# Optimization experiments

Measured on AMD Instinct MI355X. Metric: run time of the kernel, lower is better.

Reference implementation:

```python
import jax, jax.numpy as jnp
import numpy as np

B, T, P, C = 1, 256, 88, 128   # batch, time frames, 88 piano pitches, hidden_per_pitch
HEADS, WIN, NLAYERS = 4, 25, 2
HD = C // HEADS


def setup_inputs() -> dict:
    ks = jax.random.split(jax.random.key(0), 8)
    s = 0.02
    return {
        "x": jax.random.normal(ks[0], (B, T, P, C), jnp.float32),
        "condition": jax.random.normal(ks[1], (B, T, P, 2), jnp.float32),
        "mask": jax.random.uniform(ks[2], (B, T, P), jnp.float32),
        # fusion linear: Linear(hidden_per_pitch + 3, hidden_per_pitch)
        "linear_w": jax.random.normal(ks[3], (C, C + 3), jnp.float32) * s,
        "linear_b": jnp.zeros((C,), jnp.float32),
        # shared NeighborhoodAttention2D params (nn.Sequential repeats the same module)
        "qkv_w": jax.random.normal(ks[4], (3 * C, C), jnp.float32) * s,
        "qkv_b": jnp.zeros((3 * C,), jnp.float32),
        "rpb": jax.random.normal(ks[5], (HEADS, 2 * WIN - 1, 2 * WIN - 1), jnp.float32) * s,
        "proj_w": jax.random.normal(ks[6], (C, C), jnp.float32) * s,
        "proj_b": jnp.zeros((C,), jnp.float32),
    }


def _nbr_idx(n, w):
    # NATTEN edge-clamped windows: window start is clamped so every query sees w keys.
    start = jnp.clip(jnp.arange(n) - (w - 1) // 2, 0, n - w)
    idx = start[:, None] + jnp.arange(w)             # [n, w] absolute key indices
    rel = idx - jnp.arange(n)[:, None] + (w - 1)     # [n, w] rpb indices in [0, 2w-2]
    return idx, rel


def na2d(x, qkv_w, qkv_b, rpb, proj_w, proj_b):
    b, h, w_, c = x.shape
    qkv = (x @ qkv_w.T + qkv_b).reshape(b, h, w_, 3, HEADS, HD)
    q, k, v = (jnp.moveaxis(qkv[..., i, :, :], 3, 1) for i in range(3))  # [b,heads,h,w,hd]
    q = q * (HD ** -0.5)

    idx_h, rel_h = _nbr_idx(h, WIN)
    idx_w, rel_w = _nbr_idx(w_, WIN)

    def score_step(_, ki):
        kg = k[:, :, idx_h[:, ki]][:, :, :, idx_w]
        s = jnp.einsum('bhijd,bhijkd->bhijk', q, kg)
        s = s + rpb[:, rel_h[:, ki]][:, :, rel_w][None]
        return None, s

    _, scores = jax.lax.scan(score_step, None, jnp.arange(WIN))
    scores = jnp.moveaxis(scores, 0, 4)
    attn = jax.nn.softmax(scores.reshape(b, HEADS, h, w_, WIN * WIN), axis=-1)
    attn = attn.reshape(b, HEADS, h, w_, WIN, WIN)

    def out_step(acc, ki):
        vg = v[:, :, idx_h[:, ki]][:, :, :, idx_w]
        return acc + jnp.einsum('bhijk,bhijkd->bhijd', attn[..., ki, :], vg), None

    out, _ = jax.lax.scan(out_step, jnp.zeros_like(q), jnp.arange(WIN))
    out = jnp.moveaxis(out, 1, 3).reshape(b, h, w_, c)      # merge heads
    return out @ proj_w.T + proj_b


def reference(x, condition, mask, linear_w, linear_b, qkv_w, qkv_b, rpb, proj_w, proj_b):
    cat = jnp.concatenate([x, condition, mask[..., None]], axis=-1)  # [B,T,P,C+3]
    y = jax.nn.relu(cat @ linear_w.T + linear_b)
    for _ in range(NLAYERS):  # same module repeated -> shared weights
        y = na2d(y, qkv_w, qkv_b, rpb, proj_w, proj_b)
    return y
```

## Files before the change

### kernel.cpp

```cpp
#include <hip/hip_runtime.h>
#include <hip/hip_fp16.h>

#define TT 256
#define PP 88
#define CC 128
#define NN (TT * PP)
#define HEADS 4
#define HD 32
#define WIN 25
#define RPBW 49
#define RPBSZ (RPBW * RPBW)
#define SCALE 0.17677669529663687f
#define LOG2E 1.4426950408889634f
#define QSC (SCALE * LOG2E)

#define KVROW 11264
#define KVAARWS 258

#if __has_builtin(__builtin_amdgcn_exp2f)
#define EXP2(x) __builtin_amdgcn_exp2f(x)
#else
#define EXP2(x) exp2f(x)
#endif

typedef _Float16 f16;
typedef f16 f16x8 __attribute__((ext_vector_type(8)));
typedef f16 f16x8u __attribute__((ext_vector_type(8), aligned(4)));
typedef f16 f16x4 __attribute__((ext_vector_type(4)));
typedef f16 f16x4u __attribute__((ext_vector_type(4), aligned(4)));
typedef float f32x4 __attribute__((ext_vector_type(4)));
typedef float f32x4u __attribute__((ext_vector_type(4), aligned(4)));
typedef __fp16 hf16x2 __attribute__((ext_vector_type(2)));
union PkU { hf16x2 h; unsigned u; };

__global__ __launch_bounds__(256) void prep(
    const float* __restrict__ lw, const float* __restrict__ qw,
    const float* __restrict__ pw, const float* __restrict__ qb,
    const float* __restrict__ pb, const float* __restrict__ rpb,
    f16* __restrict__ lwh, f16* __restrict__ qwh, f16* __restrict__ pwh,
    f16* __restrict__ w2h, float* __restrict__ qbs, float* __restrict__ b2s,
    float* __restrict__ rpbp)
{
    const int b = blockIdx.x;
    if (b < 192) {
        int idx = b * 256 + threadIdx.x;
        if (idx < 128 * 160) {
            int r = idx / 160, c = idx - r * 160;
            lwh[idx] = (f16)(c < 131 ? lw[r * 131 + c] : 0.f);
        }
        if (idx < 384 * 128) {
            float v = qw[idx];
            if (idx < 128 * 128) v *= QSC;
            qwh[idx] = (f16)v;
        }
        if (idx < 128 * 128) pwh[idx] = (f16)pw[idx];
        if (idx < 384) qbs[idx] = qb[idx] * (idx < 128 ? QSC : 1.f);
        if (idx < 10240) rpbp[idx] = (idx < 4 * RPBSZ) ? rpb[idx] * LOG2E : 0.f;
    } else if (b < 216) {
        int t = (b - 192) * 256 + threadIdx.x;
        int i = t >> 4, l = t & 15;
        if (i < 384) {
            float s = 0.f;
            #pragma unroll
            for (int j = l * 8; j < l * 8 + 8; j++) s += qw[i * 128 + j] * pb[j];
            s += __shfl_xor(s, 1); s += __shfl_xor(s, 2);
            s += __shfl_xor(s, 4); s += __shfl_xor(s, 8);
            if (l == 0) b2s[i] = (qb[i] + s) * (i < 128 ? QSC : 1.f);
        }
    } else {
        const int bw = b - 216;
        const int m0 = (bw & 1) * 64;
        const int n0 = (bw >> 1) * 64;
        const int tid = threadIdx.x;
        const int w = tid >> 6, lane = tid & 63, quad = lane >> 4, nn = lane & 15;
        const int krow = m0 + w * 16 + nn;
        f16x8 af[4];
        #pragma unroll
        for (int ks = 0; ks < 4; ks++) {
            union { f16 e[8]; f16x8 v; } t;
            #pragma unroll
            for (int e = 0; e < 8; e++)
                t.e[e] = (f16)pw[(ks * 32 + quad * 8 + e) * 128 + krow];
            af[ks] = t.v;
        }
        f32x4 acc[4] = {};
        #pragma unroll
        for (int nt = 0; nt < 4; nt++) {
            int irow = n0 + nt * 16 + nn;
            #pragma unroll
            for (int ks = 0; ks < 4; ks++) {
                const float* qr = &qw[(size_t)irow * 128 + ks * 32 + quad * 8];
                float4 a = *(const float4*)qr, bq = *(const float4*)(qr + 4);
                PkU u0, u1, u2, u3;
                u0.h = __builtin_amdgcn_cvt_pkrtz(a.x, a.y);
                u1.h = __builtin_amdgcn_cvt_pkrtz(a.z, a.w);
                u2.h = __builtin_amdgcn_cvt_pkrtz(bq.x, bq.y);
                u3.h = __builtin_amdgcn_cvt_pkrtz(bq.z, bq.w);
                union { unsigned u[4]; f16x8 v; } bb;
                bb.u[0] = u0.u; bb.u[1] = u1.u; bb.u[2] = u2.u; bb.u[3] = u3.u;
                acc[nt] = __builtin_amdgcn_mfma_f32_16x16x32_f16(af[ks], bb.v, acc[nt], 0, 0, 0);
            }
        }
        #pragma unroll
        for (int nt = 0; nt < 4; nt++) {
            int i = n0 + nt * 16 + nn;
            float sc = (i < 128) ? QSC : 1.f;
            PkU p0, p1;
            p0.h = __builtin_amdgcn_cvt_pkrtz(acc[nt][0] * sc, acc[nt][1] * sc);
            p1.h = __builtin_amdgcn_cvt_pkrtz(acc[nt][2] * sc, acc[nt][3] * sc);
            *(uint2*)&w2h[(size_t)i * 128 + m0 + w * 16 + quad * 4] = make_uint2(p0.u, p1.u);
        }
    }
}

__global__ __launch_bounds__(256) void fusion_gemm(
    const float* __restrict__ x, const float* __restrict__ cond, const float* __restrict__ mask,
    const f16* __restrict__ lwh, const float* __restrict__ lb, f16* __restrict__ yh)
{
    __shared__ __align__(16) f16 Alds[64 * 168];
    const int m0 = blockIdx.x * 64, n0 = blockIdx.y * 64;
    const int tid = threadIdx.x;
    const int w = tid >> 6, lane = tid & 63, quad = lane >> 4, nn = lane & 15;

    {
        int r = tid >> 2, cpart = tid & 3;
        size_t pos = m0 + r;
        *(uint4*)&Alds[r * 168 + 128 + cpart * 8] = make_uint4(0, 0, 0, 0);
        const float* xr = x + pos * 128 + cpart * 32;
        #pragma unroll
        for (int t = 0; t < 4; t++) {
            float4 a = *(const float4*)(xr + t * 8);
            float4 b = *(const float4*)(xr + t * 8 + 4);
            PkU p0, p1, p2, p3;
            p0.h = __builtin_amdgcn_cvt_pkrtz(a.x, a.y);
            p1.h = __builtin_amdgcn_cvt_pkrtz(a.z, a.w);
            p2.h = __builtin_amdgcn_cvt_pkrtz(b.x, b.y);
            p3.h = __builtin_amdgcn_cvt_pkrtz(b.z, b.w);
            *(uint4*)&Alds[r * 168 + cpart * 32 + t * 8] = make_uint4(p0.u, p1.u, p2.u, p3.u);
        }
        if (cpart == 0) {
            Alds[r * 168 + 128] = (f16)cond[pos * 2];
            Alds[r * 168 + 129] = (f16)cond[pos * 2 + 1];
            Alds[r * 168 + 130] = (f16)mask[pos];
        }
    }
    __syncthreads();

    const int oc = n0 + w * 16 + nn;
    f16x8 af[5];
    #pragma unroll
    for (int ks = 0; ks < 5; ks++)
        af[ks] = *(const f16x8*)&lwh[(size_t)oc * 160 + ks * 32 + quad * 8];
    f32x4 acc[4] = {};
    #pragma unroll
    for (int ks = 0; ks < 5; ks++)
        #pragma unroll
        for (int nt = 0; nt < 4; nt++) {
            f16x8 bf = *(const f16x8*)&Alds[(nt * 16 + nn) * 168 + ks * 32 + quad * 8];
            acc[nt] = __builtin_amdgcn_mfma_f32_16x16x32_f16(af[ks], bf, acc[nt], 0, 0, 0);
        }
    float bv[4];
    #pragma unroll
    for (int r = 0; r < 4; r++) bv[r] = lb[n0 + w * 16 + quad * 4 + r];
    #pragma unroll
    for (int nt = 0; nt < 4; nt++) {
        int pos = m0 + nt * 16 + nn;
        PkU p0, p1;
        p0.h = __builtin_amdgcn_cvt_pkrtz(fmaxf(acc[nt][0] + bv[0], 0.f), fmaxf(acc[nt][1] + bv[1], 0.f));
        p1.h = __builtin_amdgcn_cvt_pkrtz(fmaxf(acc[nt][2] + bv[2], 0.f), fmaxf(acc[nt][3] + bv[3], 0.f));
        *(uint2*)&yh[(size_t)pos * 128 + n0 + w * 16 + quad * 4] = make_uint2(p0.u, p1.u);
    }
}

__global__ __launch_bounds__(256) void gemm_qkv(
    const f16* __restrict__ A, const f16* __restrict__ W, const float* __restrict__ bias,
    f16* __restrict__ qh, f16* __restrict__ kh2, f16* __restrict__ vh2)
{
    __shared__ __align__(16) f16 Alds[64 * 136];
    const int m0 = blockIdx.x * 64, n0 = blockIdx.y * 64;
    const int tid = threadIdx.x;
    const int w = tid >> 6, lane = tid & 63, quad = lane >> 4, nn = lane & 15;

    for (int i = tid; i < 1024; i += 256) {
        int r = i >> 4, c = i & 15;
        *(uint4*)&Alds[r * 136 + c * 8] = *(const uint4*)&A[(size_t)(m0 + r) * 128 + c * 8];
    }
    __syncthreads();

    const int oc = n0 + w * 16 + nn;
    f16x8 af[4];
    #pragma unroll
    for (int ks = 0; ks < 4; ks++)
        af[ks] = *(const f16x8*)&W[(size_t)oc * 128 + ks * 32 + quad * 8];
    f32x4 acc[4] = {};
    #pragma unroll
    for (int ks = 0; ks < 4; ks++)
        #pragma unroll
        for (int nt = 0; nt < 4; nt++) {
            f16x8 bf = *(const f16x8*)&Alds[(nt * 16 + nn) * 136 + ks * 32 + quad * 8];
            acc[nt] = __builtin_amdgcn_mfma_f32_16x16x32_f16(af[ks], bf, acc[nt], 0, 0, 0);
        }
    float bv[4];
    #pragma unroll
    for (int r = 0; r < 4; r++) bv[r] = bias[n0 + w * 16 + quad * 4 + r];

    if (n0 < 128) {
        #pragma unroll
        for (int nt = 0; nt < 4; nt++) {
            int pos = m0 + nt * 16 + nn;
            PkU p0, p1;
            p0.h = __builtin_amdgcn_cvt_pkrtz(acc[nt][0] + bv[0], acc[nt][1] + bv[1]);
            p1.h = __builtin_amdgcn_cvt_pkrtz(acc[nt][2] + bv[2], acc[nt][3] + bv[3]);
            *(uint2*)&qh[(size_t)pos * 128 + n0 + w * 16 + quad * 4] = make_uint2(p0.u, p1.u);
        }
    } else if (n0 < 256) {
        const int ch = n0 - 128 + w * 16 + quad * 4;
        const int hh = ch >> 5, c32 = ch & 31;
        #pragma unroll
        for (int nt = 0; nt < 4; nt++) {
            int pos = m0 + nt * 16 + nn;
            int aa = pos / 88, j = pos - aa * 88;
            PkU p0, p1;
            p0.h = __builtin_amdgcn_cvt_pkrtz(acc[nt][0] + bv[0], acc[nt][1] + bv[1]);
            p1.h = __builtin_amdgcn_cvt_pkrtz(acc[nt][2] + bv[2], acc[nt][3] + bv[3]);
            *(uint2*)&kh2[((size_t)(aa * 4 + hh) * 88 + j) * 32 + c32] = make_uint2(p0.u, p1.u);
        }
    } else {
        const int chb = n0 - 256 + w * 16 + quad * 4;
        #pragma unroll
        for (int nt = 0; nt < 4; nt++) {
            int pos = m0 + nt * 16 + nn;
            int aa = pos / 88, j = pos - aa * 88;
            size_t vb = (size_t)(aa * 4) * 2816 + (j >> 2) * 64 + (j & 3);
            #pragma unroll
            for (int r = 0; r < 4; r++) {
                int chg = chb + r;
                int hh = chg >> 5, c = chg & 31;
                vh2[vb + (size_t)hh * 2816 + (c >> 4) * 1408 + (c & 15) * 4] =
                    (f16)(acc[nt][r] + bv[r]);
            }
        }
    }
}

__global__ __launch_bounds__(256) void gemm_out(
    const f16* __restrict__ A, const f16* __restrict__ W, const float* __restrict__ bias,
    float* __restrict__ outp)
{
    __shared__ __align__(16) f16 Alds[64 * 136];
    const int m0 = blockIdx.x * 64, n0 = blockIdx.y * 64;
    const int tid = threadIdx.x;
    const int w = tid >> 6, lane = tid & 63, quad = lane >> 4, nn = lane & 15;

    for (int i = tid; i < 1024; i += 256) {
        int r = i >> 4, c = i & 15;
        *(uint4*)&Alds[r * 136 + c * 8] = *(const uint4*)&A[(size_t)(m0 + r) * 128 + c * 8];
    }
    __syncthreads();

    const int oc = n0 + w * 16 + nn;
    f16x8 af[4];
    #pragma unroll
    for (int ks = 0; ks < 4; ks++)
        af[ks] = *(const f16x8*)&W[(size_t)oc * 128 + ks * 32 + quad * 8];
    f32x4 acc[4] = {};
    #pragma unroll
    for (int ks = 0; ks < 4; ks++)
        #pragma unroll
        for (int nt = 0; nt < 4; nt++) {
            f16x8 bf = *(const f16x8*)&Alds[(nt * 16 + nn) * 136 + ks * 32 + quad * 8];
            acc[nt] = __builtin_amdgcn_mfma_f32_16x16x32_f16(af[ks], bf, acc[nt], 0, 0, 0);
        }
    float bv[4];
    #pragma unroll
    for (int r = 0; r < 4; r++) bv[r] = bias[n0 + w * 16 + quad * 4 + r];
    #pragma unroll
    for (int nt = 0; nt < 4; nt++) {
        int pos = m0 + nt * 16 + nn;
        f32x4 vv;
        #pragma unroll
        for (int r = 0; r < 4; r++) vv[r] = acc[nt][r] + bv[r];
        *(f32x4*)&outp[(size_t)pos * 128 + n0 + w * 16 + quad * 4] = vv;
    }
}

__global__ __launch_bounds__(128, 3) void attn_mfma(
    const f16* __restrict__ qh,
    const f16* __restrict__ kh2,
    const f16* __restrict__ vh2,
    const float* __restrict__ rpbp,
    f16* __restrict__ ao)
{
    const int bx = ((blockIdx.x & 7) << 3) + (blockIdx.x >> 3);
    const int i0 = bx * 4;
    const int j0 = blockIdx.y * 8;
    const int h  = blockIdx.z;
    const int tid = threadIdx.x;
    const int w = tid >> 6, lane = tid & 63;
    const int quad = lane >> 4, nn = lane & 15;

    const int ri0 = min(max(i0 - 12, 0), TT - 28);
    const int rj0 = min(max(j0 - 12, 0), PP - WIN) & ~3;

    __shared__ __align__(16) float Olds[64][28];

    int si_[2];
    unsigned pm_[2][4];
    f16x8 qf[2];
    const float* rpq[2];
    const float* rp_h = rpbp + h * RPBSZ;
    const int aa0 = ri0 + w * 14;

    #pragma unroll
    for (int q = 0; q < 2; q++) {
        int ql = q * 16 + nn;
        int qi = i0 + (ql >> 3), qj = j0 + (ql & 7);
        int si = min(max(qi - 12, 0), TT - WIN);
        int sj = min(max(qj - 12, 0), PP - WIN);
        si_[q] = si;
        unsigned cm = 0x1FFFFFFu << (sj - rj0);
        #pragma unroll
        for (int t = 0; t < 4; t++) {
            int k0 = (t >> 1) * 16 + quad * 4 + (t & 1) * 2;
            pm_[q][t] = (((cm >> k0) & 1u) ? 0xFFFFu : 0u)
                      | (((cm >> (k0 + 1)) & 1u) ? 0xFFFF0000u : 0u);
        }
        qf[q] = *(const f16x8*)&qh[(size_t)(qi * PP + qj) * 128 + h * HD + quad * 8];
        rpq[q] = rp_h + (aa0 - qi + 24) * RPBW + (rj0 - qj + 24) + quad * 4;
    }

    const int b0 = min(rj0 + nn, PP - 1);
    const int b1 = min(rj0 + 16 + nn, PP - 1);
    const f16x4 ones4 = {(f16)1.f, (f16)1.f, (f16)1.f, (f16)1.f};

    const f16* kb = kh2 + (size_t)(aa0 * 4 + h) * 2816 + quad * 8;
    const f16* vb = vh2 + (size_t)(aa0 * 4 + h) * 2816 + ((rj0 >> 2) + quad) * 64 + nn * 4;

    f32x4 O[2][2] = {};
    f32x4 lacc[2] = {};
    union PB { unsigned u[2]; f16x4 v; };
    PB pa_[2], pb_[2];
    f32x4 za_[2], zb_[2];

    int aa = aa0;
    f16x8 kf0 = *(const f16x8*)(kb + (size_t)b0 * 32);
    f16x8 kf1 = *(const f16x8*)(kb + (size_t)b1 * 32);
    f16x4 vfA0 = *(const f16x4u*)vb;
    f16x4 vfB0 = *(const f16x4u*)(vb + 256);
    f16x4 vfA1 = *(const f16x4u*)(vb + 1408);
    f16x4 vfB1 = *(const f16x4u*)(vb + 1664);
    #pragma unroll
    for (int q = 0; q < 2; q++) {
        za_[q] = *(const f32x4u*)rpq[q];
        zb_[q] = *(const f32x4u*)(rpq[q] + 16);
        rpq[q] += RPBW;
    }
    #pragma unroll
    for (int q = 0; q < 2; q++) {
        f32x4 s0 = __builtin_amdgcn_mfma_f32_16x16x32_f16(kf0, qf[q], za_[q], 0, 0, 0);
        f32x4 s1 = __builtin_amdgcn_mfma_f32_16x16x32_f16(kf1, qf[q], zb_[q], 0, 0, 0);
        bool rv = (unsigned)(aa - si_[q]) <= 24u;
        float p[8];
        #pragma unroll
        for (int r = 0; r < 4; r++) { p[r] = EXP2(s0[r]); p[r + 4] = EXP2(s1[r]); }
        PkU u0, u1, u2, u3;
        u0.h = __builtin_amdgcn_cvt_pkrtz(p[0], p[1]);
        u1.h = __builtin_amdgcn_cvt_pkrtz(p[2], p[3]);
        u2.h = __builtin_amdgcn_cvt_pkrtz(p[4], p[5]);
        u3.h = __builtin_amdgcn_cvt_pkrtz(p[6], p[7]);
        pa_[q].u[0] = rv ? (u0.u & pm_[q][0]) : 0u;
        pa_[q].u[1] = rv ? (u1.u & pm_[q][1]) : 0u;
        pb_[q].u[0] = rv ? (u2.u & pm_[q][2]) : 0u;
        pb_[q].u[1] = rv ? (u3.u & pm_[q][3]) : 0u;
    }
    kb += KVROW;
    f16x8 nkf0 = *(const f16x8*)(kb + (size_t)b0 * 32);
    f16x8 nkf1 = *(const f16x8*)(kb + (size_t)b1 * 32);

    #pragma unroll
    for (int c = 1; c < 14; ++c) {
        aa = aa0 + c;
        kf0 = nkf0; kf1 = nkf1;

        #pragma unroll
        for (int q = 0; q < 2; q++) {
            za_[q] = *(const f32x4u*)rpq[q];
            zb_[q] = *(const f32x4u*)(rpq[q] + 16);
            rpq[q] += RPBW;
        }

        __builtin_amdgcn_s_setprio(1);
        #pragma unroll
        for (int q = 0; q < 2; q++) {
            O[q][0] = __builtin_amdgcn_mfma_f32_16x16x16f16(pa_[q].v, vfA0, O[q][0], 0, 0, 0);
            O[q][0] = __builtin_amdgcn_mfma_f32_16x16x16f16(pb_[q].v, vfB0, O[q][0], 0, 0, 0);
            O[q][1] = __builtin_amdgcn_mfma_f32_16x16x16f16(pa_[q].v, vfA1, O[q][1], 0, 0, 0);
            O[q][1] = __builtin_amdgcn_mfma_f32_16x16x16f16(pb_[q].v, vfB1, O[q][1], 0, 0, 0);
            lacc[q] = __builtin_amdgcn_mfma_f32_16x16x16f16(pa_[q].v, ones4, lacc[q], 0, 0, 0);
            lacc[q] = __builtin_amdgcn_mfma_f32_16x16x16f16(pb_[q].v, ones4, lacc[q], 0, 0, 0);
        }
        __builtin_amdgcn_s_setprio(0);

        vb += KVROW;
        vfA0 = *(const f16x4u*)vb;
        vfB0 = *(const f16x4u*)(vb + 256);
        vfA1 = *(const f16x4u*)(vb + 1408);
        vfB1 = *(const f16x4u*)(vb + 1664);

        kb += KVROW;
        nkf0 = *(const f16x8*)(kb + (size_t)b0 * 32);
        nkf1 = *(const f16x8*)(kb + (size_t)b1 * 32);

        #pragma unroll
        for (int q = 0; q < 2; q++) {
            f32x4 s0 = __builtin_amdgcn_mfma_f32_16x16x32_f16(kf0, qf[q], za_[q], 0, 0, 0);
            f32x4 s1 = __builtin_amdgcn_mfma_f32_16x16x32_f16(kf1, qf[q], zb_[q], 0, 0, 0);
            bool rv = (unsigned)(aa - si_[q]) <= 24u;
            float p[8];
            #pragma unroll
            for (int r = 0; r < 4; r++) { p[r] = EXP2(s0[r]); p[r + 4] = EXP2(s1[r]); }
            PkU u0, u1, u2, u3;
            u0.h = __builtin_amdgcn_cvt_pkrtz(p[0], p[1]);
            u1.h = __builtin_amdgcn_cvt_pkrtz(p[2], p[3]);
            u2.h = __builtin_amdgcn_cvt_pkrtz(p[4], p[5]);
            u3.h = __builtin_amdgcn_cvt_pkrtz(p[6], p[7]);
            pa_[q].u[0] = rv ? (u0.u & pm_[q][0]) : 0u;
            pa_[q].u[1] = rv ? (u1.u & pm_[q][1]) : 0u;
            pb_[q].u[0] = rv ? (u2.u & pm_[q][2]) : 0u;
            pb_[q].u[1] = rv ? (u3.u & pm_[q][3]) : 0u;
        }
    }

    #pragma unroll
    for (int q = 0; q < 2; q++) {
        O[q][0] = __builtin_amdgcn_mfma_f32_16x16x16f16(pa_[q].v, vfA0, O[q][0], 0, 0, 0);
        O[q][0] = __builtin_amdgcn_mfma_f32_16x16x16f16(pb_[q].v, vfB0, O[q][0], 0, 0, 0);
        O[q][1] = __builtin_amdgcn_mfma_f32_16x16x16f16(pa_[q].v, vfA1, O[q][1], 0, 0, 0);
        O[q][1] = __builtin_amdgcn_mfma_f32_16x16x16f16(pb_[q].v, vfB1, O[q][1], 0, 0, 0);
        lacc[q] = __builtin_amdgcn_mfma_f32_16x16x16f16(pa_[q].v, ones4, lacc[q], 0, 0, 0);
        lacc[q] = __builtin_amdgcn_mfma_f32_16x16x16f16(pb_[q].v, ones4, lacc[q], 0, 0, 0);
    }

    if (w == 1) {
        float* ob = &Olds[lane][0];
        #pragma unroll
        for (int q = 0; q < 2; q++) {
            *(f32x4*)&ob[q * 12]     = O[q][0];
            *(f32x4*)&ob[q * 12 + 4] = O[q][1];
            *(f32x4*)&ob[q * 12 + 8] = lacc[q];
        }
    }
    __syncthreads();
    if (w == 0) {
        const float* ob = &Olds[lane][0];
        #pragma unroll
        for (int q = 0; q < 2; q++) {
            f32x4 o0 = O[q][0] + *(const f32x4*)&ob[q * 12];
            f32x4 o1 = O[q][1] + *(const f32x4*)&ob[q * 12 + 4];
            f32x4 la = lacc[q] + *(const f32x4*)&ob[q * 12 + 8];
            #pragma unroll
            for (int r = 0; r < 4; r++) {
                float li = 1.f / la[r];
                int ql = q * 16 + quad * 4 + r;
                int qi = i0 + (ql >> 3), qj = j0 + (ql & 7);
                size_t base = (size_t)(qi * PP + qj) * CC + h * HD;
                ao[base + nn]      = (f16)(o0[r] * li);
                ao[base + 16 + nn] = (f16)(o1[r] * li);
            }
        }
    }
}

extern "C" void kernel_launch(void* const* d_in, const int* in_sizes, int n_in,
                              void* d_out, int out_size, void* d_ws, size_t ws_size,
                              hipStream_t stream) {
    (void)in_sizes; (void)n_in; (void)out_size; (void)ws_size;
    const float* x    = (const float*)d_in[0];
    const float* cond = (const float*)d_in[1];
    const float* mask = (const float*)d_in[2];
    const float* lw   = (const float*)d_in[3];
    const float* lb   = (const float*)d_in[4];
    const float* qw   = (const float*)d_in[5];
    const float* qb   = (const float*)d_in[6];
    const float* rpb  = (const float*)d_in[7];
    const float* pw   = (const float*)d_in[8];
    const float* pb   = (const float*)d_in[9];
    float* outp       = (float*)d_out;

    float* ws   = (float*)d_ws;
    float* qbs  = ws;
    float* b2s  = qbs + 384;
    float* rpbp = b2s + 384;
    f16* lwh  = (f16*)(rpbp + 10240);
    f16* qwh  = lwh + 20480;
    f16* pwh  = qwh + 49152;
    f16* w2h  = pwh + 16384;
    f16* yh   = w2h + 49152;
    f16* qh   = yh + (size_t)NN * 128;
    f16* kh2  = qh + (size_t)NN * 128;
    f16* vh2  = kh2 + (size_t)KVAARWS * KVROW;
    f16* ao   = vh2 + (size_t)KVAARWS * KVROW;

    prep<<<228, 256, 0, stream>>>(lw, qw, pw, qb, pb, rpb, lwh, qwh, pwh, w2h, qbs, b2s, rpbp);
    fusion_gemm<<<dim3(352, 2), 256, 0, stream>>>(x, cond, mask, lwh, lb, yh);
    gemm_qkv<<<dim3(352, 6), 256, 0, stream>>>(yh, qwh, qbs, qh, kh2, vh2);
    attn_mfma<<<dim3(TT / 4, PP / 8, HEADS), 128, 0, stream>>>(qh, kh2, vh2, rpbp, ao);
    gemm_qkv<<<dim3(352, 6), 256, 0, stream>>>(ao, w2h, b2s, qh, kh2, vh2);
    attn_mfma<<<dim3(TT / 4, PP / 8, HEADS), 128, 0, stream>>>(qh, kh2, vh2, rpbp, ao);
    gemm_out<<<dim3(352, 2), 256, 0, stream>>>(ao, pwh, pb, outp);
}
```

Before: 193.7 us.

## Pre-swizzle QKV weights into MFMA fragment order and stage outputs through LDS

```diff
diff --git a/kernel.cpp b/kernel.cpp
--- a/kernel.cpp
+++ b/kernel.cpp
@@ -33,12 +33,13 @@
 typedef __fp16 hf16x2 __attribute__((ext_vector_type(2)));
 union PkU { hf16x2 h; unsigned u; };
 
+
 __global__ __launch_bounds__(256) void prep(
     const float* __restrict__ lw, const float* __restrict__ qw,
     const float* __restrict__ pw, const float* __restrict__ qb,
     const float* __restrict__ pb, const float* __restrict__ rpb,
-    f16* __restrict__ lwh, f16* __restrict__ qwh, f16* __restrict__ pwh,
-    f16* __restrict__ w2h, float* __restrict__ qbs, float* __restrict__ b2s,
+    f16* __restrict__ lwh, f16* __restrict__ qwf, f16* __restrict__ pwh,
+    f16* __restrict__ w2f, float* __restrict__ qbs, float* __restrict__ b2s,
     float* __restrict__ rpbp)
 {
     const int b = blockIdx.x;
@@ -51,7 +52,10 @@
         if (idx < 384 * 128) {
             float v = qw[idx];
             if (idx < 128 * 128) v *= QSC;
-            qwh[idx] = (f16)v;
+            int i = idx >> 7, k = idx & 127;
+            int lane = (((k & 31) >> 3) << 4) + (i & 15);
+            int faddr = (((i >> 6) << 2) + ((i >> 4) & 3)) * 2048 + (k >> 5) * 512 + lane * 8 + (k & 7);
+            qwf[faddr] = (f16)v;
         }
         if (idx < 128 * 128) pwh[idx] = (f16)pw[idx];
         if (idx < 384) qbs[idx] = qb[idx] * (idx < 128 ? QSC : 1.f);
@@ -104,11 +108,14 @@
         #pragma unroll
         for (int nt = 0; nt < 4; nt++) {
             int i = n0 + nt * 16 + nn;
+            int k = m0 + w * 16 + quad * 4;
             float sc = (i < 128) ? QSC : 1.f;
             PkU p0, p1;
             p0.h = __builtin_amdgcn_cvt_pkrtz(acc[nt][0] * sc, acc[nt][1] * sc);
             p1.h = __builtin_amdgcn_cvt_pkrtz(acc[nt][2] * sc, acc[nt][3] * sc);
-            *(uint2*)&w2h[(size_t)i * 128 + m0 + w * 16 + quad * 4] = make_uint2(p0.u, p1.u);
+            int lane2 = (((k & 31) >> 3) << 4) + (i & 15);
+            int faddr = (((i >> 6) << 2) + ((i >> 4) & 3)) * 2048 + (k >> 5) * 512 + lane2 * 8 + (k & 7);
+            *(uint2*)&w2f[faddr] = make_uint2(p0.u, p1.u);
         }
     }
 }
@@ -173,10 +180,11 @@
 }
 
 __global__ __launch_bounds__(256) void gemm_qkv(
-    const f16* __restrict__ A, const f16* __restrict__ W, const float* __restrict__ bias,
+    const f16* __restrict__ A, const f16* __restrict__ Wf, const float* __restrict__ bias,
     f16* __restrict__ qh, f16* __restrict__ kh2, f16* __restrict__ vh2)
 {
     __shared__ __align__(16) f16 Alds[64 * 136];
+    __shared__ __align__(16) f16 Rlds[64][72];
     const int m0 = blockIdx.x * 64, n0 = blockIdx.y * 64;
     const int tid = threadIdx.x;
     const int w = tid >> 6, lane = tid & 63, quad = lane >> 4, nn = lane & 15;
@@ -187,11 +195,11 @@
     }
     __syncthreads();
 
-    const int oc = n0 + w * 16 + nn;
+    const f16* wfb = Wf + ((size_t)(n0 >> 6) * 4 + w) * 2048 + lane * 8;
     f16x8 af[4];
     #pragma unroll
     for (int ks = 0; ks < 4; ks++)
-        af[ks] = *(const f16x8*)&W[(size_t)oc * 128 + ks * 32 + quad * 8];
+        af[ks] = *(const f16x8*)(wfb + ks * 512);
     f32x4 acc[4] = {};
     #pragma unroll
     for (int ks = 0; ks < 4; ks++)
@@ -204,41 +212,59 @@
     #pragma unroll
     for (int r = 0; r < 4; r++) bv[r] = bias[n0 + w * 16 + quad * 4 + r];
 
-    if (n0 < 128) {
-        #pragma unroll
-        for (int nt = 0; nt < 4; nt++) {
-            int pos = m0 + nt * 16 + nn;
+    if (n0 < 256) {
+        #pragma unroll
+        for (int nt = 0; nt < 4; nt++) {
             PkU p0, p1;
             p0.h = __builtin_amdgcn_cvt_pkrtz(acc[nt][0] + bv[0], acc[nt][1] + bv[1]);
             p1.h = __builtin_amdgcn_cvt_pkrtz(acc[nt][2] + bv[2], acc[nt][3] + bv[3]);
-            *(uint2*)&qh[(size_t)pos * 128 + n0 + w * 16 + quad * 4] = make_uint2(p0.u, p1.u);
+            *(uint2*)&Rlds[nt * 16 + nn][w * 16 + quad * 4] = make_uint2(p0.u, p1.u);
+        }
+    } else {
+        #pragma unroll
+        for (int nt = 0; nt < 4; nt++) {
+            union { f16 e[4]; uint2 u; } t;
+            #pragma unroll
+            for (int r = 0; r < 4; r++) t.e[r] = (f16)(acc[nt][r] + bv[r]);
+            *(uint2*)&Rlds[nt * 16 + nn][w * 16 + quad * 4] = t.u;
+        }
+    }
+    __syncthreads();
+
+    if (n0 < 128) {
+        #pragma unroll
+        for (int it = 0; it < 2; it++) {
+            int idx = it * 256 + tid;
+            int pl = idx >> 3, oct = idx & 7;
+            f16x8 v = *(const f16x8*)&Rlds[pl][oct * 8];
+            *(uint4*)&qh[(size_t)(m0 + pl) * 128 + n0 + oct * 8] = *(uint4*)&v;
         }
     } else if (n0 < 256) {
-        const int ch = n0 - 128 + w * 16 + quad * 4;
-        const int hh = ch >> 5, c32 = ch & 31;
-        #pragma unroll
-        for (int nt = 0; nt < 4; nt++) {
-            int pos = m0 + nt * 16 + nn;
-            int aa = pos / 88, j = pos - aa * 88;
-            PkU p0, p1;
-            p0.h = __builtin_amdgcn_cvt_pkrtz(acc[nt][0] + bv[0], acc[nt][1] + bv[1]);
-            p1.h = __builtin_amdgcn_cvt_pkrtz(acc[nt][2] + bv[2], acc[nt][3] + bv[3]);
-            *(uint2*)&kh2[((size_t)(aa * 4 + hh) * 88 + j) * 32 + c32] = make_uint2(p0.u, p1.u);
+        #pragma unroll
+        for (int it = 0; it < 2; it++) {
+            int idx = it * 256 + tid;
+            int pl = idx >> 3, oct = idx & 7;
+            f16x8 v = *(const f16x8*)&Rlds[pl][oct * 8];
+            int pos = m0 + pl, aa = pos / 88, j = pos - aa * 88;
+            int ch = n0 - 128 + oct * 8;
+            int h = ch >> 5, c32 = ch & 31;
+            *(uint4*)&kh2[((size_t)(aa * 4 + h) * 88 + j) * 32 + c32] = *(uint4*)&v;
         }
     } else {
-        const int chb = n0 - 256 + w * 16 + quad * 4;
-        #pragma unroll
-        for (int nt = 0; nt < 4; nt++) {
-            int pos = m0 + nt * 16 + nn;
-            int aa = pos / 88, j = pos - aa * 88;
-            size_t vb = (size_t)(aa * 4) * 2816 + (j >> 2) * 64 + (j & 3);
-            #pragma unroll
-            for (int r = 0; r < 4; r++) {
-                int chg = chb + r;
-                int hh = chg >> 5, c = chg & 31;
-                vh2[vb + (size_t)hh * 2816 + (c >> 4) * 1408 + (c & 15) * 4] =
-                    (f16)(acc[nt][r] + bv[r]);
-            }
+        #pragma unroll
+        for (int it = 0; it < 2; it++) {
+            int idx = it * 256 + tid;
+            int pq = idx >> 5, cp = idx & 31;
+            union { f16 e[8]; uint4 u; } t;
+            #pragma unroll
+            for (int cc = 0; cc < 2; cc++)
+                #pragma unroll
+                for (int jj = 0; jj < 4; jj++)
+                    t.e[cc * 4 + jj] = Rlds[pq * 4 + jj][cp * 2 + cc];
+            int pos = m0 + pq * 4, aa = pos / 88, j = pos - aa * 88;
+            int ch = n0 - 256 + cp * 2;
+            int h = ch >> 5, c = ch & 31, half = c >> 4, c16 = c & 15;
+            *(uint4*)&vh2[(size_t)(aa * 4 + h) * 2816 + half * 1408 + (j >> 2) * 64 + c16 * 4] = t.u;
         }
     }
 }
@@ -492,20 +518,20 @@
     float* b2s  = qbs + 384;
     float* rpbp = b2s + 384;
     f16* lwh  = (f16*)(rpbp + 10240);
-    f16* qwh  = lwh + 20480;
-    f16* pwh  = qwh + 49152;
-    f16* w2h  = pwh + 16384;
-    f16* yh   = w2h + 49152;
+    f16* qwf  = lwh + 20480;
+    f16* pwh  = qwf + 49152;
+    f16* w2f  = pwh + 16384;
+    f16* yh   = w2f + 49152;
     f16* qh   = yh + (size_t)NN * 128;
     f16* kh2  = qh + (size_t)NN * 128;
     f16* vh2  = kh2 + (size_t)KVAARWS * KVROW;
     f16* ao   = vh2 + (size_t)KVAARWS * KVROW;
 
-    prep<<<228, 256, 0, stream>>>(lw, qw, pw, qb, pb, rpb, lwh, qwh, pwh, w2h, qbs, b2s, rpbp);
+    prep<<<228, 256, 0, stream>>>(lw, qw, pw, qb, pb, rpb, lwh, qwf, pwh, w2f, qbs, b2s, rpbp);
     fusion_gemm<<<dim3(352, 2), 256, 0, stream>>>(x, cond, mask, lwh, lb, yh);
-    gemm_qkv<<<dim3(352, 6), 256, 0, stream>>>(yh, qwh, qbs, qh, kh2, vh2);
+    gemm_qkv<<<dim3(352, 6), 256, 0, stream>>>(yh, qwf, qbs, qh, kh2, vh2);
     attn_mfma<<<dim3(TT / 4, PP / 8, HEADS), 128, 0, stream>>>(qh, kh2, vh2, rpbp, ao);
-    gemm_qkv<<<dim3(352, 6), 256, 0, stream>>>(ao, w2h, b2s, qh, kh2, vh2);
+    gemm_qkv<<<dim3(352, 6), 256, 0, stream>>>(ao, w2f, b2s, qh, kh2, vh2);
     attn_mfma<<<dim3(TT / 4, PP / 8, HEADS), 128, 0, stream>>>(qh, kh2, vh2, rpbp, ao);
     gemm_out<<<dim3(352, 2), 256, 0, stream>>>(ao, pwh, pb, outp);
 }
```

Result: faster. 184.4 us (-4.8%).
